# Kernel tuning notes

Hardware: AMD Instinct MI355X
Metric: run time of the kernel (lower is better)

Reference implementation:

```python
import jax, jax.numpy as jnp
import numpy as np

E, D, H, O, K = 12, 1024, 2048, 1024, 4
HH, G1, G2 = H // 2, 256, 128
B = 4096


def _ln(x, g, b):
    # torch LayerNorm over last dim, eps=1e-5
    m = x.mean(-1, keepdims=True)
    v = ((x - m) ** 2).mean(-1, keepdims=True)
    return (x - m) * jax.lax.rsqrt(v + 1e-5) * g + b


def setup_inputs() -> dict:
    key = jax.random.key(0)
    ks = jax.random.split(key, 12)
    s = 0.02
    f32 = jnp.float32
    return {
        "x": jax.random.normal(ks[0], (B, D), f32),
        # stacked expert params (E experts)
        "ew_in": jax.random.normal(ks[1], (E, D, H), f32) * s,
        "eb_in": jnp.full((E, H), 0.1, f32),
        "ln1_g": jnp.ones((E, H), f32),
        "ln1_b": jnp.zeros((E, H), f32),
        "ew_h1": jax.random.normal(ks[2], (E, H, H), f32) * s,
        "eb_h1": jnp.full((E, H), 0.1, f32),
        "ln2_g": jnp.ones((E, H), f32),
        "ln2_b": jnp.zeros((E, H), f32),
        "ew_h2": jax.random.normal(ks[3], (E, H, HH), f32) * s,
        "eb_h2": jnp.full((E, HH), 0.1, f32),
        "ew_out": jax.random.normal(ks[4], (E, HH, O), f32) * s,
        "eb_out": jnp.zeros((E, O), f32),
        # gating network params
        "gw_in": jax.random.normal(ks[5], (D, G1), f32) * s,
        "gb_in": jnp.zeros((G1,), f32),
        "gln1_g": jnp.ones((G1,), f32),
        "gln1_b": jnp.zeros((G1,), f32),
        "gw_1": jax.random.normal(ks[6], (G1, G1), f32) * s,
        "gb_1": jnp.full((G1,), 0.1, f32),
        "gln2_g": jnp.ones((G1,), f32),
        "gln2_b": jnp.zeros((G1,), f32),
        "gw_2": jax.random.normal(ks[7], (G1, G2), f32) * s,
        "gb_2": jnp.full((G2,), 0.1, f32),
        "gw_out": jax.random.normal(ks[8], (G2, E), f32) * s,
        "gb_out": jnp.zeros((E,), f32),
        "temperature": jnp.ones((1,), f32),
    }


def _moe(x, ew_in, eb_in, ln1_g, ln1_b, ew_h1, eb_h1, ln2_g, ln2_b, ew_h2,
         eb_h2, ew_out, eb_out, gw_in, gb_in, gln1_g, gln1_b, gw_1, gb_1,
         gln2_g, gln2_b, gw_2, gb_2, gw_out, gb_out, temperature):
    # ---- gating network (eval mode: no dropout / noise) ----
    g0 = jax.nn.relu(x @ gw_in + gb_in)                                # [B,256]
    g1 = jax.nn.relu(_ln(g0, gln1_g, gln1_b)) @ gw_1 + gb_1 + g0       # residual
    g2 = jax.nn.relu(_ln(g1, gln2_g, gln2_b)) @ gw_2 + gb_2            # [B,128]
    logits = (g2 @ gw_out + gb_out) / temperature                      # [B,E]
    probs = jax.nn.softmax(logits, axis=1)
    topp, topi = jax.lax.top_k(probs, K)                               # [B,K]
    topp = topp / topp.sum(axis=1, keepdims=True)
    # ---- experts: batched over E, combined with top-k one-hot weights ----
    h0 = jax.nn.relu(jnp.einsum('bd,edh->ebh', x, ew_in) + eb_in[:, None, :])
    a1 = jax.nn.relu(_ln(h0, ln1_g[:, None, :], ln1_b[:, None, :]))
    h1 = jnp.einsum('ebh,ehg->ebg', a1, ew_h1) + eb_h1[:, None, :] + h0
    a2 = jax.nn.silu(_ln(h1, ln2_g[:, None, :], ln2_b[:, None, :]))
    h2 = jnp.einsum('ebh,ehm->ebm', a2, ew_h2) + eb_h2[:, None, :]     # [E,B,H/2]
    y = jnp.einsum('ebm,emo->ebo', h2, ew_out) + eb_out[:, None, :]    # [E,B,O]
    oh = jax.nn.one_hot(topi, E, dtype=probs.dtype)                    # [B,K,E]
    w = jnp.einsum('bk,bke->be', topp, oh)                             # combine weights
    final = jnp.einsum('be,ebo->bo', w, y)                             # [B,O]
    # ---- load-balancing loss (eval-mode path) ----
    usage = probs.mean(axis=0)                                         # [E]
    ideal = 1.0 / E
    kl = jnp.sum(ideal * (jnp.log(ideal) - jnp.log(usage + 1e-8)))
    var = jnp.sum((usage - ideal) ** 2)
    ent = -jnp.sum(usage * jnp.log(usage + 1e-8))
    ent_loss = 1.0 - ent / np.log(E).astype(np.float32)
    loss = (0.5 * kl + 0.3 * var + 0.2 * ent_loss) * 0.05
    return final, loss, probs


def reference(x, ew_in, eb_in, ln1_g, ln1_b, ew_h1, eb_h1, ln2_g, ln2_b,
              ew_h2, eb_h2, ew_out, eb_out, gw_in, gb_in, gln1_g, gln1_b,
              gw_1, gb_1, gln2_g, gln2_b, gw_2, gb_2, gw_out, gb_out,
              temperature):
    return _moe(x, ew_in, eb_in, ln1_g, ln1_b, ew_h1, eb_h1, ln2_g, ln2_b,
                ew_h2, eb_h2, ew_out, eb_out, gw_in, gb_in, gln1_g, gln1_b,
                gw_1, gb_1, gln2_g, gln2_b, gw_2, gb_2, gw_out, gb_out,
                temperature)
```

## Files before the change

kernel.cpp:

```cpp
#include <hip/hip_runtime.h>
#include <cstdint>
#include <cstddef>

typedef __bf16 bf16;
typedef __bf16 bf16x4 __attribute__((ext_vector_type(4)));
typedef __bf16 bf16x8 __attribute__((ext_vector_type(8)));
typedef float  f32x4  __attribute__((ext_vector_type(4)));

#define NE   12
#define DDIM 1024
#define HDIM 2048
#define MDIM 1024
#define ODIM 1024
#define GG1  256
#define GG2  128
#define BB   4096
#define ROWS_MAX 18432

#define GPTR(p) ((const __attribute__((address_space(1))) void*)(p))
#define LPTR(p) ((__attribute__((address_space(3))) void*)(p))

__global__ void cvt_f32_bf16(const float* __restrict__ in, bf16* __restrict__ out) {
    size_t i = ((size_t)blockIdx.x * 256 + threadIdx.x) * 4;
    float4 v = *(const float4*)(in + i);
    bf16x4 o = { (bf16)v.x, (bf16)v.y, (bf16)v.z, (bf16)v.w };
    *(bf16x4*)(out + i) = o;
}

__global__ void transpose_cvt(const float* __restrict__ in, bf16* __restrict__ out,
                              int K, int N) {
    __shared__ float tile[32][33];
    const size_t eo = (size_t)blockIdx.z * K * N;
    in  += eo;
    out += eo;
    const int n0 = blockIdx.x * 32, k0 = blockIdx.y * 32;
    const int tx = threadIdx.x, ty = threadIdx.y;
    #pragma unroll
    for (int i = 0; i < 4; ++i)
        tile[ty + i * 8][tx] = in[(size_t)(k0 + ty + i * 8) * N + n0 + tx];
    __syncthreads();
    #pragma unroll
    for (int i = 0; i < 4; ++i)
        out[(size_t)(n0 + ty + i * 8) * K + k0 + tx] = (bf16)tile[tx][ty + i * 8];
}

__global__ void route_init(int* __restrict__ tok2slot, int* __restrict__ lists,
                           int* __restrict__ counts, int* __restrict__ cursors) {
    const int i = blockIdx.x * 256 + threadIdx.x;
    if (i < BB * NE)   tok2slot[i] = -1;
    if (i < ROWS_MAX)  lists[i] = 0;
    if (i < NE)        { counts[i] = 0; cursors[i] = 0; }
}

__global__ void route_count(const float* __restrict__ wcomb, int* __restrict__ counts) {
    const int t = blockIdx.x * 256 + threadIdx.x;
    const int e = blockIdx.y;
    if (wcomb[(size_t)t * NE + e] > 0.f) atomicAdd(&counts[e], 1);
}

__global__ void route_offsets(const int* __restrict__ counts, int* __restrict__ offs) {
    if (threadIdx.x == 0) {
        int o = 0;
        for (int e = 0; e < NE; ++e) { offs[e] = o; o += (counts[e] + 127) & ~127; }
        offs[NE] = o;
    }
}

__global__ void route_assign(const float* __restrict__ wcomb, const int* __restrict__ offs,
                             int* __restrict__ cursors, int* __restrict__ lists,
                             int* __restrict__ tok2slot) {
    const int t = blockIdx.x * 256 + threadIdx.x;
    const int e = blockIdx.y;
    if (wcomb[(size_t)t * NE + e] > 0.f) {
        const int pos  = atomicAdd(&cursors[e], 1);
        const int slot = offs[e] + pos;
        lists[slot] = t;
        tok2slot[(size_t)t * NE + e] = slot;
    }
}

__global__ void gather_rows(const bf16* __restrict__ xb, const int* __restrict__ lists,
                            const int* __restrict__ offs, bf16* __restrict__ xg) {
    const int e = blockIdx.y, p = blockIdx.x;
    const int off = offs[e];
    if (p >= offs[e + 1] - off) return;
    const int slot = off + p;
    const int t = lists[slot];
    const int tid = threadIdx.x;
    *(bf16x4*)&xg[(size_t)slot * DDIM + tid * 4] =
        *(const bf16x4*)&xb[(size_t)t * DDIM + tid * 4];
}

__global__ void combine_out(const int* __restrict__ tok2slot, const float* __restrict__ wcomb,
                            const float* __restrict__ yc, float* __restrict__ out) {
    const int t = blockIdx.x, tid = threadIdx.x;
    float4 acc = { 0.f, 0.f, 0.f, 0.f };
    #pragma unroll
    for (int e = 0; e < NE; ++e) {
        const int s = tok2slot[(size_t)t * NE + e];
        if (s >= 0) {
            const float w = wcomb[(size_t)t * NE + e];
            const float4 y = *(const float4*)&yc[(size_t)s * ODIM + tid * 4];
            acc.x += w * y.x; acc.y += w * y.y; acc.z += w * y.z; acc.w += w * y.w;
        }
    }
    *(float4*)&out[(size_t)t * ODIM + tid * 4] = acc;
}

template<int EPI>
__global__ __launch_bounds__(256, 2)
void egemm(const bf16* __restrict__ A, const bf16* __restrict__ Wt,
           const float* __restrict__ bias, const bf16* __restrict__ res,
           bf16* __restrict__ Cb, float* __restrict__ Cf,
           const int* __restrict__ offs, int N, int K)
{
    const int e = blockIdx.z;
    const int off  = offs[e];
    const int cntp = offs[e + 1] - off;
    const int m0 = blockIdx.y * 128;
    if (m0 >= cntp) return;
    const int n0 = blockIdx.x * 128;

    __shared__ bf16 sA[2][128 * 32];
    __shared__ bf16 sB[2][128 * 32];
    const int tid  = threadIdx.x;
    const int lane = tid & 63;
    const int wave = tid >> 6;
    const int wr = wave >> 1, wc = wave & 1;
    const int q  = lane >> 4;
    const int lr = lane & 15;

    const bf16*  Ae  = A + (size_t)off * K;
    const bf16*  Wte = Wt + (size_t)e * N * K;
    const float* be  = bias + (size_t)e * N;

    const bf16* srcA[2];
    const bf16* srcB[2];
    int dsto[2];
    #pragma unroll
    for (int i = 0; i < 2; ++i) {
        const int ch  = i * 256 + tid;
        const int row = ch >> 2, c = ch & 3;
        const int qg  = c ^ ((row >> 1) & 3);
        srcA[i] = Ae  + (size_t)(m0 + row) * K + qg * 8;
        srcB[i] = Wte + (size_t)(n0 + row) * K + qg * 8;
        dsto[i] = (i * 256 + (tid & 192)) * 8;
    }

    f32x4 acc[4][4] = {};

    auto stage = [&](int buf, int k0) {
        #pragma unroll
        for (int i = 0; i < 2; ++i) {
            __builtin_amdgcn_global_load_lds(GPTR(srcA[i] + k0), LPTR(&sA[buf][dsto[i]]), 16, 0, 0);
            __builtin_amdgcn_global_load_lds(GPTR(srcB[i] + k0), LPTR(&sB[buf][dsto[i]]), 16, 0, 0);
        }
    };

    stage(0, 0);
    __syncthreads();

    const int NT = K >> 5;
    int cur = 0;
    for (int kt = 0; kt < NT; ++kt) {
        if (kt + 1 < NT) stage(cur ^ 1, (kt + 1) << 5);
        bf16x8 fa[4], fb[4];
        #pragma unroll
        for (int mi = 0; mi < 4; ++mi) {
            const int r = wr * 64 + mi * 16 + lr;
            const int c = q ^ ((r >> 1) & 3);
            fa[mi] = *(const bf16x8*)&sA[cur][(size_t)(r * 4 + c) * 8];
        }
        #pragma unroll
        for (int ni = 0; ni < 4; ++ni) {
            const int r = wc * 64 + ni * 16 + lr;
            const int c = q ^ ((r >> 1) & 3);
            fb[ni] = *(const bf16x8*)&sB[cur][(size_t)(r * 4 + c) * 8];
        }
        #pragma unroll
        for (int mi = 0; mi < 4; ++mi)
            #pragma unroll
            for (int ni = 0; ni < 4; ++ni)
                acc[mi][ni] = __builtin_amdgcn_mfma_f32_16x16x32_bf16(fa[mi], fb[ni], acc[mi][ni], 0, 0, 0);
        __syncthreads();
        cur ^= 1;
    }

    #pragma unroll
    for (int ni = 0; ni < 4; ++ni) {
        const int c  = n0 + wc * 64 + ni * 16 + lr;
        const float bv = be[c];
        #pragma unroll
        for (int mi = 0; mi < 4; ++mi) {
            const int rloc = wr * 64 + mi * 16 + q * 4;
            #pragma unroll
            for (int j = 0; j < 4; ++j) {
                const size_t idx = (size_t)(off + m0 + rloc + j) * N + c;
                float v = acc[mi][ni][j] + bv;
                if constexpr (EPI == 0)      { Cb[idx] = (bf16)fmaxf(v, 0.f); }
                else if constexpr (EPI == 1) { Cb[idx] = (bf16)(v + (float)res[idx]); }
                else if constexpr (EPI == 2) { Cb[idx] = (bf16)v; }
                else                         { Cf[idx] = v; }
            }
        }
    }
}

template<int ACT>
__global__ __launch_bounds__(256)
void ln_act_bf16(const bf16* __restrict__ in, const float* __restrict__ gam,
                 const float* __restrict__ bet, bf16* __restrict__ out,
                 const int* __restrict__ offs)
{
    const int e = blockIdx.y;
    const int row = blockIdx.x;
    const int off = offs[e];
    if (row >= offs[e + 1] - off) return;
    const int tid = threadIdx.x;
    const size_t base = (size_t)(off + row) * HDIM;
    const float* g = gam + (size_t)e * HDIM;
    const float* b = bet + (size_t)e * HDIM;
    bf16x8 v = *(const bf16x8*)(in + base + tid * 8);
    float x[8], s = 0.f, ss = 0.f;
    #pragma unroll
    for (int j = 0; j < 8; ++j) { x[j] = (float)v[j]; s += x[j]; ss += x[j] * x[j]; }
    #pragma unroll
    for (int o = 1; o < 64; o <<= 1) { s += __shfl_xor(s, o); ss += __shfl_xor(ss, o); }
    __shared__ float rs[4], rss[4];
    if ((tid & 63) == 0) { rs[tid >> 6] = s; rss[tid >> 6] = ss; }
    __syncthreads();
    s  = rs[0] + rs[1] + rs[2] + rs[3];
    ss = rss[0] + rss[1] + rss[2] + rss[3];
    const float mean = s * (1.f / HDIM);
    const float var  = ss * (1.f / HDIM) - mean * mean;
    const float rstd = rsqrtf(var + 1e-5f);
    bf16x8 ov;
    #pragma unroll
    for (int j = 0; j < 8; ++j) {
        const int col = tid * 8 + j;
        float y = (x[j] - mean) * rstd * g[col] + b[col];
        if constexpr (ACT == 0) y = fmaxf(y, 0.f);
        else                    y = y / (1.f + expf(-y));
        ov[j] = (bf16)y;
    }
    *(bf16x8*)(out + base + tid * 8) = ov;
}

template<int EPI>
__global__ __launch_bounds__(256)
void gemm_f32(const float* __restrict__ A, const float* __restrict__ Bm,
              const float* __restrict__ bias, const float* __restrict__ res,
              float* __restrict__ C, int M, int N, int K)
{
    __shared__ float As[64][17];
    __shared__ float Bs[16][64];
    const int tid = threadIdx.x;
    const int tx = tid & 15, ty = tid >> 4;
    const int n0 = blockIdx.x * 64, m0 = blockIdx.y * 64;
    float acc[4][4] = {};

    for (int k0 = 0; k0 < K; k0 += 16) {
        {
            const int r = tid >> 2, c = (tid & 3) * 4;
            const float4 va = *(const float4*)(A + (size_t)(m0 + r) * K + k0 + c);
            As[r][c] = va.x; As[r][c + 1] = va.y; As[r][c + 2] = va.z; As[r][c + 3] = va.w;
            const int rb = tid >> 4, cb = (tid & 15) * 4;
            *(float4*)&Bs[rb][cb] = *(const float4*)(Bm + (size_t)(k0 + rb) * N + n0 + cb);
        }
        __syncthreads();
        #pragma unroll
        for (int k = 0; k < 16; ++k) {
            const float4 b4 = *(const float4*)&Bs[k][tx * 4];
            float av[4];
            #pragma unroll
            for (int i = 0; i < 4; ++i) av[i] = As[ty * 4 + i][k];
            #pragma unroll
            for (int i = 0; i < 4; ++i) {
                acc[i][0] += av[i] * b4.x; acc[i][1] += av[i] * b4.y;
                acc[i][2] += av[i] * b4.z; acc[i][3] += av[i] * b4.w;
            }
        }
        __syncthreads();
    }

    const float4 b4 = *(const float4*)(bias + n0 + tx * 4);
    #pragma unroll
    for (int i = 0; i < 4; ++i) {
        const int r = m0 + ty * 4 + i;
        float o[4] = { acc[i][0] + b4.x, acc[i][1] + b4.y, acc[i][2] + b4.z, acc[i][3] + b4.w };
        if constexpr (EPI == 0) {
            #pragma unroll
            for (int j = 0; j < 4; ++j) o[j] = fmaxf(o[j], 0.f);
        } else if constexpr (EPI == 1) {
            const float4 r4 = *(const float4*)(res + (size_t)r * N + n0 + tx * 4);
            o[0] += r4.x; o[1] += r4.y; o[2] += r4.z; o[3] += r4.w;
        }
        float4 o4 = { o[0], o[1], o[2], o[3] };
        *(float4*)(C + (size_t)r * N + n0 + tx * 4) = o4;
    }
}

__global__ void ln_relu_f32_256(const float* __restrict__ in, const float* __restrict__ g,
                                const float* __restrict__ b, float* __restrict__ out)
{
    const int row = blockIdx.x, lane = threadIdx.x;
    const size_t base = (size_t)row * GG1;
    const float4 v = *(const float4*)(in + base + lane * 4);
    float s  = v.x + v.y + v.z + v.w;
    float ss = v.x * v.x + v.y * v.y + v.z * v.z + v.w * v.w;
    #pragma unroll
    for (int o = 1; o < 64; o <<= 1) { s += __shfl_xor(s, o); ss += __shfl_xor(ss, o); }
    const float mean = s * (1.f / GG1);
    const float var  = ss * (1.f / GG1) - mean * mean;
    const float rstd = rsqrtf(var + 1e-5f);
    const float4 g4 = *(const float4*)(g + lane * 4);
    const float4 b4 = *(const float4*)(b + lane * 4);
    float4 o4;
    o4.x = fmaxf((v.x - mean) * rstd * g4.x + b4.x, 0.f);
    o4.y = fmaxf((v.y - mean) * rstd * g4.y + b4.y, 0.f);
    o4.z = fmaxf((v.z - mean) * rstd * g4.z + b4.z, 0.f);
    o4.w = fmaxf((v.w - mean) * rstd * g4.w + b4.w, 0.f);
    *(float4*)(out + base + lane * 4) = o4;
}

__global__ void gate_head(const float* __restrict__ g2, const float* __restrict__ gwout,
                          const float* __restrict__ gbout, const float* __restrict__ temp,
                          float* __restrict__ probs_out, float* __restrict__ wout)
{
    const int row = blockIdx.x, lane = threadIdx.x;
    __shared__ float lg[NE];
    const int e = lane >> 2, part = lane & 3;
    float acc = 0.f;
    if (e < NE) {
        const float* gr = g2 + (size_t)row * GG2;
        #pragma unroll
        for (int i = 0; i < 32; ++i) {
            const int k = part * 32 + i;
            acc += gr[k] * gwout[(size_t)k * NE + e];
        }
    }
    acc += __shfl_xor(acc, 1);
    acc += __shfl_xor(acc, 2);
    if (e < NE && part == 0) lg[e] = acc + gbout[e];
    __syncthreads();
    if (lane == 0) {
        const float t = temp[0];
        float p[NE];
        float mx = -1e30f;
        #pragma unroll
        for (int i = 0; i < NE; ++i) { p[i] = lg[i] / t; mx = fmaxf(mx, p[i]); }
        float se = 0.f;
        #pragma unroll
        for (int i = 0; i < NE; ++i) { p[i] = expf(p[i] - mx); se += p[i]; }
        const float inv = 1.f / se;
        #pragma unroll
        for (int i = 0; i < NE; ++i) { p[i] *= inv; probs_out[(size_t)row * NE + i] = p[i]; }
        float qq[NE], w[NE];
        #pragma unroll
        for (int i = 0; i < NE; ++i) { qq[i] = p[i]; w[i] = 0.f; }
        float tv[4]; int ti[4]; float tsum = 0.f;
        for (int k = 0; k < 4; ++k) {
            int best = 0; float bv = qq[0];
            for (int i = 1; i < NE; ++i) if (qq[i] > bv) { bv = qq[i]; best = i; }
            tv[k] = bv; ti[k] = best; qq[best] = -1e30f; tsum += bv;
        }
        const float it = 1.f / tsum;
        for (int k = 0; k < 4; ++k) w[ti[k]] = tv[k] * it;
        #pragma unroll
        for (int i = 0; i < NE; ++i) wout[(size_t)row * NE + i] = w[i];
    }
}

__global__ void usage_mean(const float* __restrict__ probs, float* __restrict__ usage) {
    const int e = blockIdx.x, tid = threadIdx.x;
    float s = 0.f;
    for (int r = tid; r < BB; r += 256) s += probs[(size_t)r * NE + e];
    #pragma unroll
    for (int o = 1; o < 64; o <<= 1) s += __shfl_xor(s, o);
    __shared__ float ps[4];
    if ((tid & 63) == 0) ps[tid >> 6] = s;
    __syncthreads();
    if (tid == 0) usage[e] = (ps[0] + ps[1] + ps[2] + ps[3]) / (float)BB;
}

__global__ void loss_kernel(const float* __restrict__ usage, float* __restrict__ out_loss) {
    if (threadIdx.x == 0) {
        const float ideal = 1.f / 12.f;
        float kl = 0.f, var = 0.f, ent = 0.f;
        for (int e = 0; e < NE; ++e) {
            const float u = usage[e];
            kl  += ideal * (logf(ideal) - logf(u + 1e-8f));
            var += (u - ideal) * (u - ideal);
            ent -= u * logf(u + 1e-8f);
        }
        const float entl = 1.f - ent / logf(12.f);
        out_loss[0] = (0.5f * kl + 0.3f * var + 0.2f * entl) * 0.05f;
    }
}

extern "C" void kernel_launch(void* const* d_in, const int* in_sizes, int n_in,
                              void* d_out, int out_size, void* d_ws, size_t ws_size,
                              hipStream_t stream)
{
    const float* x      = (const float*)d_in[0];
    const float* ew_in  = (const float*)d_in[1];
    const float* eb_in  = (const float*)d_in[2];
    const float* ln1_g  = (const float*)d_in[3];
    const float* ln1_b  = (const float*)d_in[4];
    const float* ew_h1  = (const float*)d_in[5];
    const float* eb_h1  = (const float*)d_in[6];
    const float* ln2_g  = (const float*)d_in[7];
    const float* ln2_b  = (const float*)d_in[8];
    const float* ew_h2  = (const float*)d_in[9];
    const float* eb_h2  = (const float*)d_in[10];
    const float* ew_out = (const float*)d_in[11];
    const float* eb_out = (const float*)d_in[12];
    const float* gw_in  = (const float*)d_in[13];
    const float* gb_in  = (const float*)d_in[14];
    const float* gln1_g = (const float*)d_in[15];
    const float* gln1_b = (const float*)d_in[16];
    const float* gw_1   = (const float*)d_in[17];
    const float* gb_1   = (const float*)d_in[18];
    const float* gln2_g = (const float*)d_in[19];
    const float* gln2_b = (const float*)d_in[20];
    const float* gw_2   = (const float*)d_in[21];
    const float* gb_2   = (const float*)d_in[22];
    const float* gw_out = (const float*)d_in[23];
    const float* gb_out = (const float*)d_in[24];
    const float* temp   = (const float*)d_in[25];

    float* out_final = (float*)d_out;
    float* out_loss  = out_final + (size_t)BB * ODIM;
    float* out_probs = out_loss + 1;

    char* ws = (char*)d_ws;
    size_t off = 0;
    auto alloc = [&](size_t bytes) -> void* {
        void* p = ws + off;
        off += (bytes + 255) & ~(size_t)255;
        return p;
    };

    bf16* xb     = (bf16*)alloc((size_t)BB * DDIM * 2);
    bf16* wt_in  = (bf16*)alloc((size_t)NE * HDIM * DDIM * 2);
    bf16* wt_h1  = (bf16*)alloc((size_t)NE * HDIM * HDIM * 2);
    bf16* wt_h2  = (bf16*)alloc((size_t)NE * MDIM * HDIM * 2);
    bf16* wt_out = (bf16*)alloc((size_t)NE * ODIM * MDIM * 2);
    bf16* xg     = (bf16*)alloc((size_t)ROWS_MAX * DDIM * 2);
    bf16* regA   = (bf16*)alloc((size_t)ROWS_MAX * HDIM * 2);
    bf16* regB   = (bf16*)alloc((size_t)ROWS_MAX * HDIM * 2);
    bf16* h1     = (bf16*)alloc((size_t)ROWS_MAX * HDIM * 2);
    float* yc    = (float*)alloc((size_t)ROWS_MAX * ODIM * 4);
    bf16* h0 = regA; bf16* a2 = regA;
    bf16* a1 = regB; bf16* h2 = regB;
    float* g0    = (float*)alloc((size_t)BB * GG1 * 4);
    float* t1    = (float*)alloc((size_t)BB * GG1 * 4);
    float* g1    = (float*)alloc((size_t)BB * GG1 * 4);
    float* t2    = (float*)alloc((size_t)BB * GG1 * 4);
    float* g2b   = (float*)alloc((size_t)BB * GG2 * 4);
    float* wcomb = (float*)alloc((size_t)BB * NE * 4);
    int*   lists = (int*)alloc((size_t)ROWS_MAX * 4);
    int*   t2s   = (int*)alloc((size_t)BB * NE * 4);
    int*   counts= (int*)alloc(256);
    int*   curs  = (int*)alloc(256);
    int*   offs  = (int*)alloc(256);
    float* usage = (float*)alloc(256);

    cvt_f32_bf16<<<dim3(BB * DDIM / 1024), dim3(256), 0, stream>>>(x, xb);
    transpose_cvt<<<dim3(HDIM / 32, DDIM / 32, NE), dim3(32, 8), 0, stream>>>(ew_in,  wt_in,  DDIM, HDIM);
    transpose_cvt<<<dim3(HDIM / 32, HDIM / 32, NE), dim3(32, 8), 0, stream>>>(ew_h1,  wt_h1,  HDIM, HDIM);
    transpose_cvt<<<dim3(MDIM / 32, HDIM / 32, NE), dim3(32, 8), 0, stream>>>(ew_h2,  wt_h2,  HDIM, MDIM);
    transpose_cvt<<<dim3(ODIM / 32, MDIM / 32, NE), dim3(32, 8), 0, stream>>>(ew_out, wt_out, MDIM, ODIM);

    gemm_f32<0><<<dim3(GG1 / 64, BB / 64), dim3(256), 0, stream>>>(x,  gw_in, gb_in, nullptr, g0,  BB, GG1, DDIM);
    ln_relu_f32_256<<<dim3(BB), dim3(64), 0, stream>>>(g0, gln1_g, gln1_b, t1);
    gemm_f32<1><<<dim3(GG1 / 64, BB / 64), dim3(256), 0, stream>>>(t1, gw_1,  gb_1,  g0,      g1,  BB, GG1, GG1);
    ln_relu_f32_256<<<dim3(BB), dim3(64), 0, stream>>>(g1, gln2_g, gln2_b, t2);
    gemm_f32<2><<<dim3(GG2 / 64, BB / 64), dim3(256), 0, stream>>>(t2, gw_2,  gb_2,  nullptr, g2b, BB, GG2, GG1);
    gate_head<<<dim3(BB), dim3(64), 0, stream>>>(g2b, gw_out, gb_out, temp, out_probs, wcomb);
    usage_mean<<<dim3(NE), dim3(256), 0, stream>>>(out_probs, usage);
    loss_kernel<<<dim3(1), dim3(64), 0, stream>>>(usage, out_loss);

    route_init<<<dim3((BB * NE + 255) / 256), dim3(256), 0, stream>>>(t2s, lists, counts, curs);
    route_count<<<dim3(BB / 256, NE), dim3(256), 0, stream>>>(wcomb, counts);
    route_offsets<<<dim3(1), dim3(64), 0, stream>>>(counts, offs);
    route_assign<<<dim3(BB / 256, NE), dim3(256), 0, stream>>>(wcomb, offs, curs, lists, t2s);
    gather_rows<<<dim3(BB, NE), dim3(256), 0, stream>>>(xb, lists, offs, xg);

    egemm<0><<<dim3(HDIM / 128, BB / 128, NE), dim3(256), 0, stream>>>(
        xg, wt_in, eb_in, nullptr, h0, nullptr, offs, HDIM, DDIM);
    ln_act_bf16<0><<<dim3(BB, NE), dim3(256), 0, stream>>>(h0, ln1_g, ln1_b, a1, offs);
    egemm<1><<<dim3(HDIM / 128, BB / 128, NE), dim3(256), 0, stream>>>(
        a1, wt_h1, eb_h1, h0, h1, nullptr, offs, HDIM, HDIM);
    ln_act_bf16<1><<<dim3(BB, NE), dim3(256), 0, stream>>>(h1, ln2_g, ln2_b, a2, offs);
    egemm<2><<<dim3(MDIM / 128, BB / 128, NE), dim3(256), 0, stream>>>(
        a2, wt_h2, eb_h2, nullptr, h2, nullptr, offs, MDIM, HDIM);
    egemm<3><<<dim3(ODIM / 128, BB / 128, NE), dim3(256), 0, stream>>>(
        h2, wt_out, eb_out, nullptr, nullptr, yc, offs, ODIM, MDIM);

    combine_out<<<dim3(BB), dim3(256), 0, stream>>>(t2s, wcomb, yc, out_final);
}
```

Measured before the change: 983.0 us.

## Enlarge expert GEMM tiles to 256x256 with 4-stage LDS pipeline

The expert grouped GEMM moves from 128x128 tiles on 4 waves to 256x256 tiles on 8 waves. It replaces the double-buffered loop with a 4-slot ring that prefetches three k-steps ahead, split into four interleaved load parts, and raises wave priority around the MFMA bursts. Routing padding grows to 256 rows to match the new M tile, and ROWS_MAX increases to fit. The aims are more data reuse per tile and better hiding of global-load latency, at the cost of 64KB of LDS, higher register pressure, more wasted padded rows, and fewer blocks for small experts.

```diff
diff --git a/kernel.cpp b/kernel.cpp
--- a/kernel.cpp
+++ b/kernel.cpp
@@ -15,7 +15,7 @@
 #define GG1  256
 #define GG2  128
 #define BB   4096
-#define ROWS_MAX 18432
+#define ROWS_MAX 19456
 
 #define GPTR(p) ((const __attribute__((address_space(1))) void*)(p))
 #define LPTR(p) ((__attribute__((address_space(3))) void*)(p))
@@ -61,7 +61,7 @@
 __global__ void route_offsets(const int* __restrict__ counts, int* __restrict__ offs) {
     if (threadIdx.x == 0) {
         int o = 0;
-        for (int e = 0; e < NE; ++e) { offs[e] = o; o += (counts[e] + 127) & ~127; }
+        for (int e = 0; e < NE; ++e) { offs[e] = o; o += (counts[e] + 255) & ~255; }
         offs[NE] = o;
     }
 }
@@ -108,7 +108,7 @@
 }
 
 template<int EPI>
-__global__ __launch_bounds__(256, 2)
+__global__ __launch_bounds__(512, 2)
 void egemm(const bf16* __restrict__ A, const bf16* __restrict__ Wt,
            const float* __restrict__ bias, const bf16* __restrict__ res,
            bf16* __restrict__ Cb, float* __restrict__ Cf,
@@ -117,16 +117,17 @@
     const int e = blockIdx.z;
     const int off  = offs[e];
     const int cntp = offs[e + 1] - off;
-    const int m0 = blockIdx.y * 128;
+    const int m0 = blockIdx.y * 256;
     if (m0 >= cntp) return;
-    const int n0 = blockIdx.x * 128;
-
-    __shared__ bf16 sA[2][128 * 32];
-    __shared__ bf16 sB[2][128 * 32];
+    const int n0 = blockIdx.x * 256;
+
+    __shared__ bf16 sA[4][256 * 32];
+    __shared__ bf16 sB[4][256 * 32];
+
     const int tid  = threadIdx.x;
     const int lane = tid & 63;
-    const int wave = tid >> 6;
-    const int wr = wave >> 1, wc = wave & 1;
+    const int wid  = tid >> 6;
+    const int wm = wid >> 2, wn = wid & 3;
     const int q  = lane >> 4;
     const int lr = lane & 15;
 
@@ -134,65 +135,111 @@
     const bf16*  Wte = Wt + (size_t)e * N * K;
     const float* be  = bias + (size_t)e * N;
 
-    const bf16* srcA[2];
-    const bf16* srcB[2];
-    int dsto[2];
+    const bf16* srcA[2]; const bf16* srcB[2]; int dsto[2];
     #pragma unroll
     for (int i = 0; i < 2; ++i) {
-        const int ch  = i * 256 + tid;
-        const int row = ch >> 2, c = ch & 3;
-        const int qg  = c ^ ((row >> 1) & 3);
-        srcA[i] = Ae  + (size_t)(m0 + row) * K + qg * 8;
-        srcB[i] = Wte + (size_t)(n0 + row) * K + qg * 8;
-        dsto[i] = (i * 256 + (tid & 192)) * 8;
-    }
-
-    f32x4 acc[4][4] = {};
-
-    auto stage = [&](int buf, int k0) {
-        #pragma unroll
-        for (int i = 0; i < 2; ++i) {
-            __builtin_amdgcn_global_load_lds(GPTR(srcA[i] + k0), LPTR(&sA[buf][dsto[i]]), 16, 0, 0);
-            __builtin_amdgcn_global_load_lds(GPTR(srcB[i] + k0), LPTR(&sB[buf][dsto[i]]), 16, 0, 0);
-        }
+        const int c = i * 512 + tid;
+        const int row = c >> 2, s = c & 3;
+        const int gs = s ^ ((row >> 1) & 3);
+        srcA[i] = Ae  + (size_t)(m0 + row) * K + gs * 8;
+        srcB[i] = Wte + (size_t)(n0 + row) * K + gs * 8;
+        dsto[i] = (i * 512 + (tid & ~63)) * 8;
+    }
+
+    auto stage_part = [&](int slot, int kt, int p) {
+        const int k0 = kt << 5;
+        if (p == 0)      __builtin_amdgcn_global_load_lds(GPTR(srcA[0] + k0), LPTR(&sA[slot][dsto[0]]), 16, 0, 0);
+        else if (p == 1) __builtin_amdgcn_global_load_lds(GPTR(srcA[1] + k0), LPTR(&sA[slot][dsto[1]]), 16, 0, 0);
+        else if (p == 2) __builtin_amdgcn_global_load_lds(GPTR(srcB[0] + k0), LPTR(&sB[slot][dsto[0]]), 16, 0, 0);
+        else             __builtin_amdgcn_global_load_lds(GPTR(srcB[1] + k0), LPTR(&sB[slot][dsto[1]]), 16, 0, 0);
     };
 
-    stage(0, 0);
-    __syncthreads();
-
+    f32x4 acc[8][4] = {};
     const int NT = K >> 5;
-    int cur = 0;
+
+    #pragma unroll
+    for (int t = 0; t < 3; ++t) {
+        #pragma unroll
+        for (int p = 0; p < 4; ++p) stage_part(t, t, p);
+    }
+
+    bf16x8 fa[4], fb[4];
+
     for (int kt = 0; kt < NT; ++kt) {
-        if (kt + 1 < NT) stage(cur ^ 1, (kt + 1) << 5);
-        bf16x8 fa[4], fb[4];
-        #pragma unroll
-        for (int mi = 0; mi < 4; ++mi) {
-            const int r = wr * 64 + mi * 16 + lr;
-            const int c = q ^ ((r >> 1) & 3);
-            fa[mi] = *(const bf16x8*)&sA[cur][(size_t)(r * 4 + c) * 8];
-        }
-        #pragma unroll
-        for (int ni = 0; ni < 4; ++ni) {
-            const int r = wc * 64 + ni * 16 + lr;
-            const int c = q ^ ((r >> 1) & 3);
-            fb[ni] = *(const bf16x8*)&sB[cur][(size_t)(r * 4 + c) * 8];
-        }
-        #pragma unroll
-        for (int mi = 0; mi < 4; ++mi)
-            #pragma unroll
-            for (int ni = 0; ni < 4; ++ni)
-                acc[mi][ni] = __builtin_amdgcn_mfma_f32_16x16x32_bf16(fa[mi], fb[ni], acc[mi][ni], 0, 0, 0);
-        __syncthreads();
-        cur ^= 1;
+        const int slot = kt & 3;
+        const bf16* a_s = &sA[slot][0];
+        const bf16* b_s = &sB[slot][0];
+        asm volatile("s_waitcnt vmcnt(8)" ::: "memory");
+        __builtin_amdgcn_s_barrier();
+        __builtin_amdgcn_sched_barrier(0);
+
+        const bool pf = (kt + 3) < NT;
+        const int pslot = (kt + 3) & 3;
+
+        #pragma unroll
+        for (int f = 0; f < 4; ++f) {
+            const int r = wm * 128 + f * 16 + lr;
+            fa[f] = *(const bf16x8*)(a_s + r * 32 + (q ^ ((r >> 1) & 3)) * 8);
+        }
+        #pragma unroll
+        for (int g = 0; g < 2; ++g) {
+            const int r = wn * 64 + g * 16 + lr;
+            fb[g] = *(const bf16x8*)(b_s + r * 32 + (q ^ ((r >> 1) & 3)) * 8);
+        }
+        if (pf) stage_part(pslot, kt + 3, 0);
+        __builtin_amdgcn_s_setprio(1);
+        #pragma unroll
+        for (int f = 0; f < 4; ++f)
+            #pragma unroll
+            for (int g = 0; g < 2; ++g)
+                acc[f][g] = __builtin_amdgcn_mfma_f32_16x16x32_bf16(fa[f], fb[g], acc[f][g], 0, 0, 0);
+        __builtin_amdgcn_s_setprio(0);
+
+        #pragma unroll
+        for (int g = 0; g < 2; ++g) {
+            const int r = wn * 64 + 32 + g * 16 + lr;
+            fb[2 + g] = *(const bf16x8*)(b_s + r * 32 + (q ^ ((r >> 1) & 3)) * 8);
+        }
+        if (pf) stage_part(pslot, kt + 3, 1);
+        __builtin_amdgcn_s_setprio(1);
+        #pragma unroll
+        for (int f = 0; f < 4; ++f)
+            #pragma unroll
+            for (int g = 0; g < 2; ++g)
+                acc[f][2 + g] = __builtin_amdgcn_mfma_f32_16x16x32_bf16(fa[f], fb[2 + g], acc[f][2 + g], 0, 0, 0);
+        __builtin_amdgcn_s_setprio(0);
+
+        #pragma unroll
+        for (int f = 0; f < 4; ++f) {
+            const int r = wm * 128 + 64 + f * 16 + lr;
+            fa[f] = *(const bf16x8*)(a_s + r * 32 + (q ^ ((r >> 1) & 3)) * 8);
+        }
+        if (pf) stage_part(pslot, kt + 3, 2);
+        __builtin_amdgcn_s_setprio(1);
+        #pragma unroll
+        for (int f = 0; f < 4; ++f)
+            #pragma unroll
+            for (int g = 0; g < 2; ++g)
+                acc[4 + f][g] = __builtin_amdgcn_mfma_f32_16x16x32_bf16(fa[f], fb[g], acc[4 + f][g], 0, 0, 0);
+        __builtin_amdgcn_s_setprio(0);
+
+        if (pf) stage_part(pslot, kt + 3, 3);
+        __builtin_amdgcn_s_setprio(1);
+        #pragma unroll
+        for (int f = 0; f < 4; ++f)
+            #pragma unroll
+            for (int g = 0; g < 2; ++g)
+                acc[4 + f][2 + g] = __builtin_amdgcn_mfma_f32_16x16x32_bf16(fa[f], fb[2 + g], acc[4 + f][2 + g], 0, 0, 0);
+        __builtin_amdgcn_s_setprio(0);
     }
 
     #pragma unroll
     for (int ni = 0; ni < 4; ++ni) {
-        const int c  = n0 + wc * 64 + ni * 16 + lr;
+        const int c  = n0 + wn * 64 + ni * 16 + lr;
         const float bv = be[c];
         #pragma unroll
-        for (int mi = 0; mi < 4; ++mi) {
-            const int rloc = wr * 64 + mi * 16 + q * 4;
+        for (int mi = 0; mi < 8; ++mi) {
+            const int rloc = wm * 128 + mi * 16 + q * 4;
             #pragma unroll
             for (int j = 0; j < 4; ++j) {
                 const size_t idx = (size_t)(off + m0 + rloc + j) * N + c;
@@ -487,15 +534,15 @@
     route_assign<<<dim3(BB / 256, NE), dim3(256), 0, stream>>>(wcomb, offs, curs, lists, t2s);
     gather_rows<<<dim3(BB, NE), dim3(256), 0, stream>>>(xb, lists, offs, xg);
 
-    egemm<0><<<dim3(HDIM / 128, BB / 128, NE), dim3(256), 0, stream>>>(
+    egemm<0><<<dim3(HDIM / 256, BB / 256, NE), dim3(512), 0, stream>>>(
         xg, wt_in, eb_in, nullptr, h0, nullptr, offs, HDIM, DDIM);
     ln_act_bf16<0><<<dim3(BB, NE), dim3(256), 0, stream>>>(h0, ln1_g, ln1_b, a1, offs);
-    egemm<1><<<dim3(HDIM / 128, BB / 128, NE), dim3(256), 0, stream>>>(
+    egemm<1><<<dim3(HDIM / 256, BB / 256, NE), dim3(512), 0, stream>>>(
         a1, wt_h1, eb_h1, h0, h1, nullptr, offs, HDIM, HDIM);
     ln_act_bf16<1><<<dim3(BB, NE), dim3(256), 0, stream>>>(h1, ln2_g, ln2_b, a2, offs);
-    egemm<2><<<dim3(MDIM / 128, BB / 128, NE), dim3(256), 0, stream>>>(
+    egemm<2><<<dim3(MDIM / 256, BB / 256, NE), dim3(512), 0, stream>>>(
         a2, wt_h2, eb_h2, nullptr, h2, nullptr, offs, MDIM, HDIM);
-    egemm<3><<<dim3(ODIM / 128, BB / 128, NE), dim3(256), 0, stream>>>(
+    egemm<3><<<dim3(ODIM / 256, BB / 256, NE), dim3(512), 0, stream>>>(
         h2, wt_out, eb_out, nullptr, nullptr, yc, offs, ODIM, MDIM);
 
     combine_out<<<dim3(BB), dim3(256), 0, stream>>>(t2s, wcomb, yc, out_final);
```

After: 1.095 ms. 1.11x slower.
